# Optimization experiments

Measured on AMD Instinct MI355X. Metric: run time of the kernel, lower is better.

Reference implementation:

```python
import jax, jax.numpy as jnp
import numpy as np

B, P, G, C = 64, 5000, 300, 20   # images, preds/img, gt/img, num classes
INPUT_SIZE = 512.0
IOU_THRESH = 0.5


def setup_inputs() -> dict:
    key = jax.random.key(0)
    k1, k2, k3, k4, k5, k6, k7 = jax.random.split(key, 7)
    # predictions: [x1,y1,x2,y2,score,cls], boxes normalized to [0,1]
    pxy = jax.random.uniform(k1, (B, P, 2), minval=0.0, maxval=0.8)
    pwh = jax.random.uniform(k2, (B, P, 2), minval=0.02, maxval=0.2)
    score = jax.random.uniform(k3, (B, P, 1))
    pcls = jax.random.randint(k4, (B, P, 1), 0, C).astype(jnp.float32)
    output = jnp.concatenate([pxy, pxy + pwh, score, pcls], axis=-1)
    # ground truth: [x1,y1,x2,y2,cls]
    txy = jax.random.uniform(k5, (B, G, 2), minval=0.0, maxval=0.8)
    twh = jax.random.uniform(k6, (B, G, 2), minval=0.02, maxval=0.2)
    tcls = jax.random.randint(k7, (B, G, 1), 0, C).astype(jnp.float32)
    labels = jnp.concatenate([txy, txy + twh, tcls], axis=-1)
    return {"output": output, "labels": labels}


def reference(output, labels):
    scale = jnp.array([INPUT_SIZE, INPUT_SIZE, INPUT_SIZE, INPUT_SIZE], dtype=output.dtype)

    def match_image(preds, targets):  # preds [P,6], targets [G,5]
        tcls = targets[:, 4]
        tboxes = targets[:, :4] * scale                     # [G,4]
        tarea = (tboxes[:, 2] - tboxes[:, 0]) * (tboxes[:, 3] - tboxes[:, 1])

        def step(detected, pred):
            pbox = pred[:4] * scale
            lt = jnp.maximum(pbox[:2], tboxes[:, :2])       # [G,2]
            rb = jnp.minimum(pbox[2:], tboxes[:, 2:])
            wh = jnp.clip(rb - lt, 0.0)
            inter = wh[:, 0] * wh[:, 1]
            parea = (pbox[2] - pbox[0]) * (pbox[3] - pbox[1])
            ious = inter / (parea + tarea - inter)          # [G]
            cls_mask = tcls == pred[5]
            masked = jnp.where(cls_mask, ious, -1.0)
            bi = jnp.argmax(masked)                          # greedy argmax over same-class gt
            match = ((pred[4] > 0)
                     & jnp.any(cls_mask)
                     & (masked[bi] > IOU_THRESH)
                     & (~detected[bi]))                      # sequential dedup
            detected = detected.at[bi].set(detected[bi] | match)
            return detected, match

        _, correct = jax.lax.scan(step, jnp.zeros(tboxes.shape[0], dtype=bool), preds)
        return correct                                       # [P] bool

    correct = jax.vmap(match_image)(output, labels).astype(output.dtype)  # [B,P]
    # stats: (correct flag, score, predicted class) per prediction; tcls per image
    stats = jnp.stack([correct, output[:, :, 4], output[:, :, 5]], axis=-1)  # [B,P,3]
    tcls = labels[:, :, 4]                                                    # [B,G]
    return stats, tcls
```

## Files before the change

### kernel.cpp

```cpp
#include <hip/hip_runtime.h>
#include <cstdint>

#define B 64
#define P 5000
#define G 300
#define C 20
#define SCALE_F 512.0f
#define IOU_TH 0.5f
#define NSPLIT 4
#define PCHUNK ((P + NSPLIT - 1) / NSPLIT)
#define NTA 512
#define SPT ((PCHUNK + NTA - 1) / NTA)

#pragma clang fp contract(off)

__global__ __launch_bounds__(NTA) void match_kernel(
    const float* __restrict__ preds,
    const float* __restrict__ labels,
    float* __restrict__ out_stats,
    float* __restrict__ out_tcls,
    unsigned int* __restrict__ gfirstp,
    short* __restrict__ gbest)
{
    const int s = blockIdx.x;
    const int b = blockIdx.y;
    const int tid = threadIdx.x;

    __shared__ float4 sb[G];
    __shared__ float  sa[G];
    __shared__ short  ssi[G];
    __shared__ short  cls_s[G];
    __shared__ int    so[C + 1];
    __shared__ int    cnt[C];
    __shared__ int    pcnt[C];
    __shared__ unsigned short psorted[PCHUNK];

    const float* lab = labels + (size_t)b * G * 5;
    const float* prd = preds + (size_t)b * P * 6;
    const int pbase = s * PCHUNK;

    if (tid < C) { cnt[tid] = 0; pcnt[tid] = 0; }
    for (int t = tid; t < G; t += NTA) {
        float c = lab[t * 5 + 4];
        cls_s[t] = (short)(int)c;
        if (s == 0) out_tcls[b * G + t] = c;
    }
    __syncthreads();

    for (int t = tid; t < G; t += NTA) atomicAdd(&cnt[cls_s[t]], 1);
    #pragma unroll
    for (int k = 0; k < SPT; ++k) {
        int p = pbase + k * NTA + tid;
        if (p < pbase + PCHUNK && p < P) {
            float score = prd[p * 6 + 4];
            float fcls  = prd[p * 6 + 5];
            atomicAdd(&pcnt[(int)fcls], 1);
            size_t op = (size_t)b * P + p;
            out_stats[op * 3 + 1] = score;
            out_stats[op * 3 + 2] = fcls;
        }
    }
    __syncthreads();

    if (tid == 0) {
        int a = 0;
        for (int c = 0; c < C; ++c) { so[c] = a; a += cnt[c]; }
        so[C] = a;
    }
    if (tid == 64) {
        int a = 0;
        for (int c = 0; c < C; ++c) { int v = pcnt[c]; pcnt[c] = a; a += v; }
    }
    __syncthreads();

    for (int t = tid; t < G; t += NTA) {
        short c = cls_s[t];
        int rank = 0;
        for (int u = 0; u < t; ++u) rank += (cls_s[u] == c) ? 1 : 0;
        int pos = so[c] + rank;
        float x1 = lab[t * 5 + 0] * SCALE_F;
        float y1 = lab[t * 5 + 1] * SCALE_F;
        float x2 = lab[t * 5 + 2] * SCALE_F;
        float y2 = lab[t * 5 + 3] * SCALE_F;
        sb[pos] = make_float4(x1, y1, x2, y2);
        sa[pos] = (x2 - x1) * (y2 - y1);
        ssi[pos] = (short)t;
    }
    #pragma unroll
    for (int k = 0; k < SPT; ++k) {
        int p = pbase + k * NTA + tid;
        if (p < pbase + PCHUNK && p < P) {
            int c = (int)prd[p * 6 + 5];
            int pos = atomicAdd(&pcnt[c], 1);
            psorted[pos] = (unsigned short)p;
        }
    }
    __syncthreads();

    #pragma unroll
    for (int k = 0; k < SPT; ++k) {
        int slot = k * NTA + tid;
        if (slot >= PCHUNK) continue;
        int p = psorted[slot];
        const float* pr = prd + p * 6;
        float px1 = pr[0] * SCALE_F;
        float py1 = pr[1] * SCALE_F;
        float px2 = pr[2] * SCALE_F;
        float py2 = pr[3] * SCALE_F;
        float score = pr[4];
        int c = (int)pr[5];
        float parea = (px2 - px1) * (py2 - py1);

        int lo = so[c], hi = so[c + 1];
        float best = -1.0f;
        int bi = -1;
        for (int j = lo; j < hi; ++j) {
            float4 tb = sb[j];
            float lx = fmaxf(px1, tb.x);
            float ly = fmaxf(py1, tb.y);
            float rx = fminf(px2, tb.z);
            float ry = fminf(py2, tb.w);
            float w = fmaxf(rx - lx, 0.0f);
            float h = fmaxf(ry - ly, 0.0f);
            float inter = w * h;
            float uni = (parea + sa[j]) - inter;
            float iou = inter / uni;
            if (iou > best) { best = iou; bi = ssi[j]; }
        }

        bool eligible = (score > 0.0f) && (hi > lo) && (best > IOU_TH);
        gbest[(size_t)b * P + p] = eligible ? (short)bi : (short)-1;
        if (eligible) atomicMin(&gfirstp[b * G + bi], (unsigned int)p);
    }
}

__global__ __launch_bounds__(256) void resolve_kernel(
    const unsigned int* __restrict__ gfirstp,
    const short* __restrict__ gbest,
    float* __restrict__ out_stats)
{
    int i = blockIdx.x * 256 + threadIdx.x;
    if (i >= B * P) return;
    int b = i / P;
    int p = i - b * P;
    int bi = gbest[i];
    float corr = (bi >= 0 && gfirstp[b * G + bi] == (unsigned int)p) ? 1.0f : 0.0f;
    out_stats[(size_t)i * 3 + 0] = corr;
}

extern "C" void kernel_launch(void* const* d_in, const int* in_sizes, int n_in,
                              void* d_out, int out_size, void* d_ws, size_t ws_size,
                              hipStream_t stream) {
    const float* output = (const float*)d_in[0];
    const float* labels = (const float*)d_in[1];

    float* out_stats = (float*)d_out;
    float* out_tcls  = (float*)d_out + (size_t)B * P * 3;

    unsigned int* gfirstp = (unsigned int*)d_ws;
    short* gbest          = (short*)(gfirstp + B * G);

    hipMemsetAsync(gfirstp, 0xFF, (size_t)B * G * 4, stream);

    dim3 grid(NSPLIT, B);
    match_kernel<<<grid, NTA, 0, stream>>>(output, labels, out_stats, out_tcls,
                                           gfirstp, gbest);
    resolve_kernel<<<(B * P + 255) / 256, 256, 0, stream>>>(gfirstp, gbest, out_stats);
}
```

Baseline: 77.30 us.

## Replace global atomicMin with per-block shared firstp and drop memset

```diff
diff --git a/kernel.cpp b/kernel.cpp
--- a/kernel.cpp
+++ b/kernel.cpp
@@ -11,15 +11,14 @@
 #define PCHUNK ((P + NSPLIT - 1) / NSPLIT)
 #define NTA 512
 #define SPT ((PCHUNK + NTA - 1) / NTA)
+#define SENT 0x7FFFFFFF
 
 #pragma clang fp contract(off)
 
 __global__ __launch_bounds__(NTA) void match_kernel(
     const float* __restrict__ preds,
     const float* __restrict__ labels,
-    float* __restrict__ out_stats,
-    float* __restrict__ out_tcls,
-    unsigned int* __restrict__ gfirstp,
+    int* __restrict__ blockfp,
     short* __restrict__ gbest)
 {
     const int s = blockIdx.x;
@@ -33,6 +32,7 @@
     __shared__ int    so[C + 1];
     __shared__ int    cnt[C];
     __shared__ int    pcnt[C];
+    __shared__ int    firstp[G];
     __shared__ unsigned short psorted[PCHUNK];
 
     const float* lab = labels + (size_t)b * G * 5;
@@ -41,9 +41,8 @@
 
     if (tid < C) { cnt[tid] = 0; pcnt[tid] = 0; }
     for (int t = tid; t < G; t += NTA) {
-        float c = lab[t * 5 + 4];
-        cls_s[t] = (short)(int)c;
-        if (s == 0) out_tcls[b * G + t] = c;
+        cls_s[t] = (short)(int)lab[t * 5 + 4];
+        firstp[t] = SENT;
     }
     __syncthreads();
 
@@ -51,14 +50,8 @@
     #pragma unroll
     for (int k = 0; k < SPT; ++k) {
         int p = pbase + k * NTA + tid;
-        if (p < pbase + PCHUNK && p < P) {
-            float score = prd[p * 6 + 4];
-            float fcls  = prd[p * 6 + 5];
-            atomicAdd(&pcnt[(int)fcls], 1);
-            size_t op = (size_t)b * P + p;
-            out_stats[op * 3 + 1] = score;
-            out_stats[op * 3 + 2] = fcls;
-        }
+        if (p < pbase + PCHUNK)
+            atomicAdd(&pcnt[(int)prd[p * 6 + 5]], 1);
     }
     __syncthreads();
 
@@ -89,7 +82,7 @@
     #pragma unroll
     for (int k = 0; k < SPT; ++k) {
         int p = pbase + k * NTA + tid;
-        if (p < pbase + PCHUNK && p < P) {
+        if (p < pbase + PCHUNK) {
             int c = (int)prd[p * 6 + 5];
             int pos = atomicAdd(&pcnt[c], 1);
             psorted[pos] = (unsigned short)p;
@@ -130,22 +123,51 @@
 
         bool eligible = (score > 0.0f) && (hi > lo) && (best > IOU_TH);
         gbest[(size_t)b * P + p] = eligible ? (short)bi : (short)-1;
-        if (eligible) atomicMin(&gfirstp[b * G + bi], (unsigned int)p);
+        if (eligible) atomicMin(&firstp[bi], p);
     }
+    __syncthreads();
+
+    for (int t = tid; t < G; t += NTA)
+        blockfp[((size_t)b * NSPLIT + s) * G + t] = firstp[t];
 }
 
-__global__ __launch_bounds__(256) void resolve_kernel(
-    const unsigned int* __restrict__ gfirstp,
+__global__ __launch_bounds__(1024) void resolve_kernel(
+    const float* __restrict__ preds,
+    const float* __restrict__ labels,
+    const int* __restrict__ blockfp,
     const short* __restrict__ gbest,
-    float* __restrict__ out_stats)
+    float* __restrict__ out_stats,
+    float* __restrict__ out_tcls)
 {
-    int i = blockIdx.x * 256 + threadIdx.x;
-    if (i >= B * P) return;
-    int b = i / P;
-    int p = i - b * P;
-    int bi = gbest[i];
-    float corr = (bi >= 0 && gfirstp[b * G + bi] == (unsigned int)p) ? 1.0f : 0.0f;
-    out_stats[(size_t)i * 3 + 0] = corr;
+    const int s = blockIdx.x;
+    const int b = blockIdx.y;
+    const int tid = threadIdx.x;
+
+    __shared__ int lf[G];
+
+    if (tid < G) {
+        const int* fp = blockfp + (size_t)b * NSPLIT * G + tid;
+        int m = fp[0];
+        m = min(m, fp[G]);
+        m = min(m, fp[2 * G]);
+        m = min(m, fp[3 * G]);
+        lf[tid] = m;
+        if (s == 0) out_tcls[b * G + tid] = labels[((size_t)b * G + tid) * 5 + 4];
+    }
+    __syncthreads();
+
+    const int pbase = s * PCHUNK;
+    #pragma unroll
+    for (int k = 0; k < 2; ++k) {
+        int p = pbase + k * 1024 + tid;
+        if (p >= pbase + PCHUNK) continue;
+        size_t ip = (size_t)b * P + p;
+        int bi = gbest[ip];
+        float corr = (bi >= 0 && lf[bi] == p) ? 1.0f : 0.0f;
+        out_stats[ip * 3 + 0] = corr;
+        out_stats[ip * 3 + 1] = preds[ip * 6 + 4];
+        out_stats[ip * 3 + 2] = preds[ip * 6 + 5];
+    }
 }
 
 extern "C" void kernel_launch(void* const* d_in, const int* in_sizes, int n_in,
@@ -157,13 +179,11 @@
     float* out_stats = (float*)d_out;
     float* out_tcls  = (float*)d_out + (size_t)B * P * 3;
 
-    unsigned int* gfirstp = (unsigned int*)d_ws;
-    short* gbest          = (short*)(gfirstp + B * G);
-
-    hipMemsetAsync(gfirstp, 0xFF, (size_t)B * G * 4, stream);
+    int* blockfp = (int*)d_ws;
+    short* gbest = (short*)(blockfp + (size_t)B * NSPLIT * G);
 
     dim3 grid(NSPLIT, B);
-    match_kernel<<<grid, NTA, 0, stream>>>(output, labels, out_stats, out_tcls,
-                                           gfirstp, gbest);
-    resolve_kernel<<<(B * P + 255) / 256, 256, 0, stream>>>(gfirstp, gbest, out_stats);
+    match_kernel<<<grid, NTA, 0, stream>>>(output, labels, blockfp, gbest);
+    resolve_kernel<<<grid, 1024, 0, stream>>>(output, labels, blockfp, gbest,
+                                              out_stats, out_tcls);
 }
```

After: 76.19 us. Within noise of the previous version (-1.4%).
